# Performance work log

Hardware: AMD Instinct MI355X
Metric: run time of the kernel (lower is better)

## Reference

```python
import jax, jax.numpy as jnp
import numpy as np


def setup_inputs() -> dict:
    key = jax.random.key(0)
    ks = jax.random.split(key, 12)
    Tq, Tk, B, H = 1024, 1024, 8, 1024
    inp = {
        "inputs_q": jax.random.normal(ks[0], (Tq, B, H), jnp.float32),
        "inputs_kv": jax.random.normal(ks[1], (Tk, B, H), jnp.float32),
        "w_q": jax.random.normal(ks[2], (H, H), jnp.float32) * 0.02,
        "b_q": jnp.zeros((H,), jnp.float32),
        "w_kv": jax.random.normal(ks[3], (2 * H, H), jnp.float32) * 0.02,
        "b_kv": jnp.zeros((2 * H,), jnp.float32),
        "w_o": jax.random.normal(ks[4], (H, H), jnp.float32) * 0.02,
        "b_o": jnp.zeros((H,), jnp.float32),
        # BatchEnsemble rank-1 factors, initialized near 1
        "r_q": 1.0 + 0.05 * jax.random.normal(ks[5], (B, H), jnp.float32),
        "s_q": 1.0 + 0.05 * jax.random.normal(ks[6], (B, H), jnp.float32),
        "r_kv": 1.0 + 0.05 * jax.random.normal(ks[7], (B, H), jnp.float32),
        "s_kv": 1.0 + 0.05 * jax.random.normal(ks[8], (B, 2 * H), jnp.float32),
        "heads": 16,
    }
    return inp


def be_linear(x, w, b, r, s):
    # x: [T,B,Hin], w: [Hout,Hin], r: [B,Hin], s: [B,Hout]
    return jnp.einsum('tbh,oh->tbo', x * r, w) * s + b


def reference(inputs_q, inputs_kv, w_q, b_q, w_kv, b_kv, w_o, b_o,
              r_q, s_q, r_kv, s_kv, heads):
    Tq, B, H = inputs_q.shape
    Tk = inputs_kv.shape[0]
    hd = H // heads
    scale = hd ** -0.5

    q = be_linear(inputs_q, w_q, b_q, r_q, s_q)          # [Tq,B,H]
    kv = be_linear(inputs_kv, w_kv, b_kv, r_kv, s_kv)    # [Tk,B,2H]

    queries = q.reshape(Tq, B * heads, hd)
    kv = kv.reshape(Tk, B * heads, 2, hd)                # layout: head x {k,v} x hd
    keys = kv[:, :, 0, :]
    values = kv[:, :, 1, :]

    scores = jnp.einsum('qnd,knd->nqk', queries, keys) * scale  # [B*heads,Tq,Tk]
    probs = jax.nn.softmax(scores.astype(jnp.float32), axis=-1).astype(scores.dtype)
    # dropout_prob = 0 / eval: dropout is identity
    ctx = jnp.einsum('nqk,knd->qnd', probs, values).reshape(Tq, B, H)
    out = jnp.einsum('tbh,oh->tbo', ctx, w_o) + b_o      # [Tq,B,H]
    return out
```

## Files before the change

kernel.cpp:

```cpp
#include <hip/hip_runtime.h>
#include <stdint.h>

typedef unsigned short u16;
typedef __bf16 bf16x8 __attribute__((ext_vector_type(8)));
typedef float f32x4 __attribute__((ext_vector_type(4)));

typedef __attribute__((address_space(3))) void lds_void;
typedef const __attribute__((address_space(1))) void gbl_void;
#define GLD_LDS16(g, l) __builtin_amdgcn_global_load_lds((gbl_void*)(g), (lds_void*)(l), 16, 0, 0)

#define BAR_RELAX() asm volatile("s_waitcnt vmcnt(4)\n\ts_barrier" ::: "memory")
#define BAR_FULL()  asm volatile("s_waitcnt vmcnt(0)\n\ts_barrier" ::: "memory")

__device__ __forceinline__ u16 f2bf(float f) {
  unsigned u = __float_as_uint(f);
  u += 0x7fffu + ((u >> 16) & 1u);
  return (u16)(u >> 16);
}

__device__ __forceinline__ unsigned pk2bf(float a, float b) {
  unsigned au = __float_as_uint(a) + 0x8000u;
  unsigned bu = __float_as_uint(b) + 0x8000u;
  return __builtin_amdgcn_perm(bu, au, 0x07060302u);
}

__global__ void k_convert_all(const float* __restrict__ inq, const float* __restrict__ r_q,
                              const float* __restrict__ inkv, const float* __restrict__ r_kv,
                              const float* __restrict__ w_q, const float* __restrict__ w_kv,
                              const float* __restrict__ w_o,
                              u16* __restrict__ Xq, u16* __restrict__ Xkv,
                              u16* __restrict__ Wq, u16* __restrict__ Wkv,
                              u16* __restrict__ Wo) {
#pragma unroll 1
  for (int blk = blockIdx.x; blk < 20480; blk += 2560) {
    const float* src; const float* r = nullptr; u16* dst; int base;
    if (blk < 8192)       { src = inq;  r = r_q;  dst = Xq;  base = 0; }
    else if (blk < 16384) { src = inkv; r = r_kv; dst = Xkv; base = 8192; }
    else if (blk < 17408) { src = w_q;  dst = Wq;  base = 16384; }
    else if (blk < 19456) { src = w_kv; dst = Wkv; base = 17408; }
    else                  { src = w_o;  dst = Wo;  base = 19456; }
    int i4 = ((blk - base) * 256 + threadIdx.x) * 4;
    float4 xv = *(const float4*)(src + i4);
    if (r) {
      int rb = ((i4 >> 10) & 7) * 1024 + (i4 & 1023);
      float4 rv = *(const float4*)(r + rb);
      xv.x *= rv.x; xv.y *= rv.y; xv.z *= rv.z; xv.w *= rv.w;
    }
    unsigned long long pk = (unsigned long long)pk2bf(xv.x, xv.y)
        | ((unsigned long long)pk2bf(xv.z, xv.w) << 32);
    *(unsigned long long*)(dst + i4) = pk;
  }
}

template <int MODE>
__device__ __forceinline__ void gemm_tile(const u16* __restrict__ A, const u16* __restrict__ B,
                                          void* __restrict__ Cout, const float* __restrict__ s,
                                          const float* __restrict__ bias, int N, int K,
                                          float postscale, int bx, int by,
                                          u16* As, u16* Bs, int tid,
                                          u16* __restrict__ vt, int h) {
  const int w = tid >> 6, lane = tid & 63;
  const int quad = lane >> 4, l16 = lane & 15;
  const int n0 = bx * 128, m0 = by * 128;
  const int wm = (w & 1) * 64, wn = (w >> 1) * 64;

  f32x4 acc[4][4] = {};

  int srow[2], scol[2];
#pragma unroll
  for (int i = 0; i < 2; ++i) {
    int p = (w * 2 + i) * 64 + lane;
    int row = p >> 2;
    int cb = (p & 3) ^ ((row >> 1) & 3);
    srow[i] = row; scol[i] = cb * 8;
  }
  int offA[4], offB[4];
#pragma unroll
  for (int t = 0; t < 4; ++t) {
    int ra = wm + t * 16 + l16;
    offA[t] = ra * 32 + ((quad ^ ((ra >> 1) & 3)) * 8);
    int rb = wn + t * 16 + l16;
    offB[t] = rb * 32 + ((quad ^ ((rb >> 1) & 3)) * 8);
  }

#pragma unroll
  for (int st = 0; st < 2; ++st)
#pragma unroll
    for (int i = 0; i < 2; ++i) {
      GLD_LDS16(A + (size_t)(m0 + srow[i]) * K + st * 32 + scol[i],
                As + st * 4096 + (w * 2 + i) * 512);
      GLD_LDS16(B + (size_t)(n0 + srow[i]) * K + st * 32 + scol[i],
                Bs + st * 4096 + (w * 2 + i) * 512);
    }

  int cur = 0, nxt = 2;
#pragma unroll 1
  for (int k0 = 0; k0 < K; k0 += 32) {
    if (k0 + 32 >= K) BAR_FULL(); else BAR_RELAX();

    if (k0 + 64 < K) {
#pragma unroll
      for (int i = 0; i < 2; ++i) {
        GLD_LDS16(A + (size_t)(m0 + srow[i]) * K + (k0 + 64) + scol[i],
                  As + nxt * 4096 + (w * 2 + i) * 512);
        GLD_LDS16(B + (size_t)(n0 + srow[i]) * K + (k0 + 64) + scol[i],
                  Bs + nxt * 4096 + (w * 2 + i) * 512);
      }
    }
    const u16* Ac = As + cur * 4096;
    const u16* Bc = Bs + cur * 4096;
    bf16x8 af[4], bfr[4];
#pragma unroll
    for (int mt = 0; mt < 4; ++mt) af[mt] = *(const bf16x8*)(Ac + offA[mt]);
#pragma unroll
    for (int nt = 0; nt < 4; ++nt) bfr[nt] = *(const bf16x8*)(Bc + offB[nt]);
#pragma unroll
    for (int mt = 0; mt < 4; ++mt)
#pragma unroll
      for (int nt = 0; nt < 4; ++nt)
        acc[mt][nt] = __builtin_amdgcn_mfma_f32_16x16x32_bf16(bfr[nt], af[mt], acc[mt][nt], 0, 0, 0);
    cur = (cur == 2) ? 0 : cur + 1;
    nxt = (nxt == 2) ? 0 : nxt + 1;
  }

  if (MODE == 0) {
#pragma unroll
    for (int mt = 0; mt < 4; ++mt) {
      const int m = m0 + wm + mt * 16 + l16;
      const size_t rowb = (size_t)m * N;
      const float* srw = s + (m & 7) * N;
#pragma unroll
      for (int nt = 0; nt < 4; ++nt) {
        const int nb = n0 + wn + nt * 16 + quad * 4;
        float4 sv = *(const float4*)(srw + nb);
        float4 bv = *(const float4*)(bias + nb);
        f32x4 a = acc[mt][nt];
        unsigned long long pk =
            (unsigned long long)pk2bf((a[0] * sv.x + bv.x) * postscale,
                                      (a[1] * sv.y + bv.y) * postscale)
          | ((unsigned long long)pk2bf((a[2] * sv.z + bv.z) * postscale,
                                       (a[3] * sv.w + bv.w) * postscale) << 32);
        *(unsigned long long*)((u16*)Cout + rowb + nb) = pk;
      }
    }
  } else if (MODE == 1) {
#pragma unroll
    for (int mt = 0; mt < 4; ++mt) {
      const int m = m0 + wm + mt * 16 + l16;
      const size_t rowb = (size_t)m * N;
#pragma unroll
      for (int nt = 0; nt < 4; ++nt) {
        const int nb = n0 + wn + nt * 16 + quad * 4;
        float4 bv = *(const float4*)(bias + nb);
        f32x4 a = acc[mt][nt];
        float4 o = {a[0] + bv.x, a[1] + bv.y, a[2] + bv.z, a[3] + bv.w};
        *(float4*)((float*)Cout + rowb + nb) = o;
      }
    }
  } else {
    __syncthreads();
    if (wn == 0) {
#pragma unroll
      for (int mt = 0; mt < 4; ++mt) {
        const int m = m0 + wm + mt * 16 + l16;
        const int b = m & 7, tk = m >> 3;
        u16* krow = (u16*)Cout + ((size_t)(tk * 128 + b * 16 + h)) * 64;
        const float* srw = s + (m & 7) * N;
#pragma unroll
        for (int nt = 0; nt < 4; ++nt) {
          const int nb = n0 + nt * 16 + quad * 4;
          float4 sv = *(const float4*)(srw + nb);
          float4 bv = *(const float4*)(bias + nb);
          f32x4 a = acc[mt][nt];
          unsigned long long pk =
              (unsigned long long)pk2bf(a[0] * sv.x + bv.x, a[1] * sv.y + bv.y)
            | ((unsigned long long)pk2bf(a[2] * sv.z + bv.z, a[3] * sv.w + bv.w) << 32);
          *(unsigned long long*)(krow + nt * 16 + quad * 4) = pk;
        }
      }
    } else {
      u16* L = As + (w - 2) * 4608;
#pragma unroll
      for (int mt = 0; mt < 4; ++mt) {
        const int m = m0 + wm + mt * 16 + l16;
        const int b = m & 7;
        const int tkl = (mt * 16 + l16) >> 3;
        const float* srw = s + (m & 7) * N;
#pragma unroll
        for (int nt = 0; nt < 4; ++nt) {
          const int nb = n0 + 64 + nt * 16 + quad * 4;
          float4 sv = *(const float4*)(srw + nb);
          float4 bv = *(const float4*)(bias + nb);
          f32x4 a = acc[mt][nt];
          const int dl = nt * 16 + quad * 4;
          L[(dl + 0) * 72 + b * 8 + tkl] = f2bf(a[0] * sv.x + bv.x);
          L[(dl + 1) * 72 + b * 8 + tkl] = f2bf(a[1] * sv.y + bv.y);
          L[(dl + 2) * 72 + b * 8 + tkl] = f2bf(a[2] * sv.z + bv.z);
          L[(dl + 3) * 72 + b * 8 + tkl] = f2bf(a[3] * sv.w + bv.w);
        }
      }
      asm volatile("s_waitcnt lgkmcnt(0)" ::: "memory");
      const int tk0 = by * 16 + (wm >> 3);
#pragma unroll
      for (int it = 0; it < 8; ++it) {
        const int dloc = it * 8 + (lane >> 3);
        const int b = lane & 7;
        bf16x8 vchunk = *(const bf16x8*)(L + dloc * 72 + b * 8);
        *(bf16x8*)(vt + ((size_t)((b * 16 + h) * 64 + dloc)) * 1024 + tk0) = vchunk;
      }
    }
  }
}

__global__ void k_gemm_qkv(const u16* __restrict__ Xq, const u16* __restrict__ Wq,
                           u16* __restrict__ qout, const float* __restrict__ s_q,
                           const float* __restrict__ b_q, float qscale,
                           const u16* __restrict__ Xkv, const u16* __restrict__ Wkv,
                           u16* __restrict__ kbuf, const float* __restrict__ s_kv,
                           const float* __restrict__ b_kv, u16* __restrict__ vt) {
  __shared__ __align__(16) u16 As[3 * 4096];
  __shared__ __align__(16) u16 Bs[3 * 4096];
  const int blk = blockIdx.x;
  const int xcd = blk & 7;
  const int slot = blk >> 3;
  const int bx = slot % 24;
  const int by = xcd * 8 + slot / 24;
  if (bx < 8)
    gemm_tile<0>(Xq, Wq, qout, s_q, b_q, 1024, 1024, qscale, bx, by, As, Bs,
                 threadIdx.x, nullptr, 0);
  else
    gemm_tile<2>(Xkv, Wkv, kbuf, s_kv, b_kv, 2048, 1024, 1.0f, bx - 8, by, As, Bs,
                 threadIdx.x, vt, bx - 8);
}

__global__ void k_gemm_o(const u16* __restrict__ A, const u16* __restrict__ B,
                         float* __restrict__ Cout, const float* __restrict__ bias) {
  __shared__ __align__(16) u16 As[3 * 4096];
  __shared__ __align__(16) u16 Bs[3 * 4096];
  const int blk = blockIdx.x;
  const int xcd = blk & 7;
  const int slot = blk >> 3;
  const int bx = slot % 8;
  const int by = xcd * 8 + slot / 8;
  gemm_tile<1>(A, B, Cout, nullptr, bias, 1024, 1024, 1.0f, bx, by, As, Bs,
               threadIdx.x, nullptr, 0);
}

__global__ __launch_bounds__(256, 3) void k_attn(const u16* __restrict__ qb,
                                                 const u16* __restrict__ kb,
                                                 const u16* __restrict__ vtb,
                                                 u16* __restrict__ ctx) {
  __shared__ __align__(16) u16 Ks[2][4096];
  __shared__ __align__(16) u16 Vts[2][4096];
  __shared__ __align__(16) u16 Ps[4][32 * 72];

  const int tid = threadIdx.x;
  const int w = tid >> 6, lane = tid & 63;
  const int quad = lane >> 4, l16 = lane & 15;
  const int n = blockIdx.x & 127;
  const int q0 = (blockIdx.x >> 7) << 7;
  const int qw = q0 + w * 32;

  bf16x8 bq[2][2];
#pragma unroll
  for (int g = 0; g < 2; ++g)
#pragma unroll
    for (int ks = 0; ks < 2; ++ks)
      bq[g][ks] = *(const bf16x8*)(qb + ((size_t)(qw + g * 16 + l16) * 128 + n) * 64 + ks * 32 + quad * 8);

  const bool isK = (w < 2);
  const int wv = w & 1;
  const u16* gbase[4];
  u16* lbase[4];
#pragma unroll
  for (int i = 0; i < 4; ++i) {
    int p = (wv * 4 + i) * 64 + lane;
    int r = p >> 3;
    int scb = ((p & 7) ^ (r & 7)) * 8;
    if (isK) {
      gbase[i] = kb + ((size_t)r * 128 + n) * 64 + scb;
      lbase[i] = &Ks[0][(wv * 4 + i) * 512];
    } else {
      gbase[i] = vtb + ((size_t)n * 64 + r) * 1024 + scb;
      lbase[i] = &Vts[0][(wv * 4 + i) * 512];
    }
  }
  const size_t gstep = isK ? 8192 : 1;
  const int lstep = 4096;

  float l_i[2] = {0.f, 0.f};
  f32x4 accO[2][4] = {};
  u16* myP = Ps[w];

#pragma unroll
  for (int i = 0; i < 4; ++i) GLD_LDS16(gbase[i], lbase[i]);

#pragma unroll 1
  for (int tk0 = 0; tk0 < 1024; tk0 += 64) {
    const int cur = (tk0 >> 6) & 1;
    __syncthreads();
    if (tk0 < 960) {
      size_t goff = (size_t)(tk0 + 64) * gstep;
#pragma unroll
      for (int i = 0; i < 4; ++i)
        GLD_LDS16(gbase[i] + goff, lbase[i] + (cur ^ 1) * lstep);
    }
    const u16* Kc = Ks[cur];
    const u16* Vc = Vts[cur];

    f32x4 accS[2][4] = {};
#pragma unroll
    for (int mt = 0; mt < 4; ++mt) {
      int r = mt * 16 + l16;
#pragma unroll
      for (int ks = 0; ks < 2; ++ks) {
        bf16x8 ak = *(const bf16x8*)(Kc + r * 64 + (((ks * 4 + quad) ^ (r & 7)) << 3));
#pragma unroll
        for (int g = 0; g < 2; ++g)
          accS[g][mt] = __builtin_amdgcn_mfma_f32_16x16x32_bf16(ak, bq[g][ks], accS[g][mt], 0, 0, 0);
      }
    }

#pragma unroll
    for (int g = 0; g < 2; ++g) {
      float pv[16];
      float ss = 0.f;
#pragma unroll
      for (int mt = 0; mt < 4; ++mt)
#pragma unroll
        for (int rg = 0; rg < 4; ++rg) {
          float p = __builtin_amdgcn_exp2f(accS[g][mt][rg]);
          pv[mt * 4 + rg] = p;
          ss += p;
        }
      ss += __shfl_xor(ss, 16);
      ss += __shfl_xor(ss, 32);
      l_i[g] += ss;
      const int prow = (g * 16 + l16) * 72;
#pragma unroll
      for (int mt = 0; mt < 4; ++mt) {
        unsigned long long pk = (unsigned long long)pk2bf(pv[mt * 4 + 0], pv[mt * 4 + 1])
            | ((unsigned long long)pk2bf(pv[mt * 4 + 2], pv[mt * 4 + 3]) << 32);
        *(unsigned long long*)(myP + prow + mt * 16 + quad * 4) = pk;
      }
    }

    bf16x8 bp[2][2];
#pragma unroll
    for (int g = 0; g < 2; ++g)
#pragma unroll
      for (int ks = 0; ks < 2; ++ks)
        bp[g][ks] = *(const bf16x8*)(myP + (g * 16 + l16) * 72 + ks * 32 + quad * 8);
#pragma unroll
    for (int dt = 0; dt < 4; ++dt) {
      int r = dt * 16 + l16;
#pragma unroll
      for (int ks = 0; ks < 2; ++ks) {
        bf16x8 av = *(const bf16x8*)(Vc + r * 64 + (((ks * 4 + quad) ^ (r & 7)) << 3));
#pragma unroll
        for (int g = 0; g < 2; ++g)
          accO[g][dt] = __builtin_amdgcn_mfma_f32_16x16x32_bf16(av, bp[g][ks], accO[g][dt], 0, 0, 0);
      }
    }
  }

#pragma unroll
  for (int g = 0; g < 2; ++g) {
    float inv = 1.f / l_i[g];
    const size_t obase = ((size_t)(qw + g * 16 + l16) * 128 + n) * 64;
#pragma unroll
    for (int dt = 0; dt < 4; ++dt) {
      unsigned long long pk = (unsigned long long)pk2bf(accO[g][dt][0] * inv, accO[g][dt][1] * inv)
          | ((unsigned long long)pk2bf(accO[g][dt][2] * inv, accO[g][dt][3] * inv) << 32);
      *(unsigned long long*)(ctx + obase + dt * 16 + quad * 4) = pk;
    }
  }
}

extern "C" void kernel_launch(void* const* d_in, const int* in_sizes, int n_in,
                              void* d_out, int out_size, void* d_ws, size_t ws_size,
                              hipStream_t stream) {
  const float* inq  = (const float*)d_in[0];
  const float* inkv = (const float*)d_in[1];
  const float* w_q  = (const float*)d_in[2];
  const float* b_q  = (const float*)d_in[3];
  const float* w_kv = (const float*)d_in[4];
  const float* b_kv = (const float*)d_in[5];
  const float* w_o  = (const float*)d_in[6];
  const float* b_o  = (const float*)d_in[7];
  const float* r_q  = (const float*)d_in[8];
  const float* s_q  = (const float*)d_in[9];
  const float* r_kv = (const float*)d_in[10];
  const float* s_kv = (const float*)d_in[11];

  const size_t MEG = 1024 * 1024;
  u16* ws    = (u16*)d_ws;
  u16* Xq    = ws;
  u16* Xkv   = ws + 8 * MEG;
  u16* Wq    = ws + 16 * MEG;
  u16* Wkv   = ws + 17 * MEG;
  u16* Wo    = ws + 19 * MEG;
  u16* qbuf  = ws + 20 * MEG;
  u16* kbuf  = ws + 28 * MEG;
  u16* vt    = ws + 36 * MEG;
  u16* ctx   = Xq;

  k_convert_all<<<2560, 256, 0, stream>>>(inq, r_q, inkv, r_kv, w_q, w_kv, w_o,
                                          Xq, Xkv, Wq, Wkv, Wo);

  const float QSCALE = 0.125f * 1.44269504088896340736f;
  k_gemm_qkv<<<1536, 256, 0, stream>>>(Xq, Wq, qbuf, s_q, b_q, QSCALE,
                                       Xkv, Wkv, kbuf, s_kv, b_kv, vt);
  k_attn<<<1024, 256, 0, stream>>>(qbuf, kbuf, vt, ctx);
  k_gemm_o<<<512, 256, 0, stream>>>(ctx, Wo, (float*)d_out, b_o);
}
```

Measured before the change: 290.0 us.

## Use 256x128 tiles in the fused QKV projection GEMM

The QKV projection GEMM now uses 256-row by 128-column output tiles, with 8x4 MFMA accumulators per wave, instead of 128x128, which halves the grid to 768 blocks. The A-tile loads, the barrier wait count and the V-transpose epilogue (LDS staging stride and store pattern) are adjusted to match. The aim is to reuse the B tile across more rows and cut global and LDS traffic per flop. In exchange it uses more registers and LDS, which may lower occupancy, and fewer blocks may leave the wave tail less balanced.

```diff
diff --git a/kernel.cpp b/kernel.cpp
--- a/kernel.cpp
+++ b/kernel.cpp
@@ -9,8 +9,9 @@
 typedef const __attribute__((address_space(1))) void gbl_void;
 #define GLD_LDS16(g, l) __builtin_amdgcn_global_load_lds((gbl_void*)(g), (lds_void*)(l), 16, 0, 0)
 
-#define BAR_RELAX() asm volatile("s_waitcnt vmcnt(4)\n\ts_barrier" ::: "memory")
-#define BAR_FULL()  asm volatile("s_waitcnt vmcnt(0)\n\ts_barrier" ::: "memory")
+#define BAR_RELAX()  asm volatile("s_waitcnt vmcnt(4)\n\ts_barrier" ::: "memory")
+#define BAR_RELAX6() asm volatile("s_waitcnt vmcnt(6)\n\ts_barrier" ::: "memory")
+#define BAR_FULL()   asm volatile("s_waitcnt vmcnt(0)\n\ts_barrier" ::: "memory")
 
 __device__ __forceinline__ u16 f2bf(float f) {
   unsigned u = __float_as_uint(f);
@@ -53,69 +54,81 @@
 }
 
 template <int MODE>
-__device__ __forceinline__ void gemm_tile(const u16* __restrict__ A, const u16* __restrict__ B,
-                                          void* __restrict__ Cout, const float* __restrict__ s,
-                                          const float* __restrict__ bias, int N, int K,
-                                          float postscale, int bx, int by,
-                                          u16* As, u16* Bs, int tid,
-                                          u16* __restrict__ vt, int h) {
+__device__ __forceinline__ void gemm_tile_w128(const u16* __restrict__ A, const u16* __restrict__ B,
+                                               void* __restrict__ Cout, const float* __restrict__ s,
+                                               const float* __restrict__ bias, int N, int K,
+                                               float postscale, int bx, int by,
+                                               u16* As, u16* Bs, int tid,
+                                               u16* __restrict__ vt, int h) {
   const int w = tid >> 6, lane = tid & 63;
   const int quad = lane >> 4, l16 = lane & 15;
-  const int n0 = bx * 128, m0 = by * 128;
-  const int wm = (w & 1) * 64, wn = (w >> 1) * 64;
-
-  f32x4 acc[4][4] = {};
-
-  int srow[2], scol[2];
+  const int n0 = bx * 128, m0 = by * 256;
+  const int wm = (w & 1) * 128, wn = (w >> 1) * 64;
+
+  f32x4 acc[8][4] = {};
+
+  int arow[4], acol[4];
+#pragma unroll
+  for (int i = 0; i < 4; ++i) {
+    int p = (w * 4 + i) * 64 + lane;
+    arow[i] = p >> 2;
+    acol[i] = ((p & 3) ^ ((arow[i] >> 1) & 3)) * 8;
+  }
+  int brow[2], bcol[2];
 #pragma unroll
   for (int i = 0; i < 2; ++i) {
     int p = (w * 2 + i) * 64 + lane;
-    int row = p >> 2;
-    int cb = (p & 3) ^ ((row >> 1) & 3);
-    srow[i] = row; scol[i] = cb * 8;
-  }
-  int offA[4], offB[4];
-#pragma unroll
-  for (int t = 0; t < 4; ++t) {
+    brow[i] = p >> 2;
+    bcol[i] = ((p & 3) ^ ((brow[i] >> 1) & 3)) * 8;
+  }
+  int offA[8], offB[4];
+#pragma unroll
+  for (int t = 0; t < 8; ++t) {
     int ra = wm + t * 16 + l16;
     offA[t] = ra * 32 + ((quad ^ ((ra >> 1) & 3)) * 8);
+  }
+#pragma unroll
+  for (int t = 0; t < 4; ++t) {
     int rb = wn + t * 16 + l16;
     offB[t] = rb * 32 + ((quad ^ ((rb >> 1) & 3)) * 8);
   }
 
 #pragma unroll
-  for (int st = 0; st < 2; ++st)
-#pragma unroll
-    for (int i = 0; i < 2; ++i) {
-      GLD_LDS16(A + (size_t)(m0 + srow[i]) * K + st * 32 + scol[i],
-                As + st * 4096 + (w * 2 + i) * 512);
-      GLD_LDS16(B + (size_t)(n0 + srow[i]) * K + st * 32 + scol[i],
+  for (int st = 0; st < 2; ++st) {
+#pragma unroll
+    for (int i = 0; i < 4; ++i)
+      GLD_LDS16(A + (size_t)(m0 + arow[i]) * K + st * 32 + acol[i],
+                As + st * 8192 + (w * 4 + i) * 512);
+#pragma unroll
+    for (int i = 0; i < 2; ++i)
+      GLD_LDS16(B + (size_t)(n0 + brow[i]) * K + st * 32 + bcol[i],
                 Bs + st * 4096 + (w * 2 + i) * 512);
-    }
+  }
 
   int cur = 0, nxt = 2;
 #pragma unroll 1
   for (int k0 = 0; k0 < K; k0 += 32) {
-    if (k0 + 32 >= K) BAR_FULL(); else BAR_RELAX();
+    if (k0 + 32 >= K) BAR_FULL(); else BAR_RELAX6();
 
     if (k0 + 64 < K) {
 #pragma unroll
-      for (int i = 0; i < 2; ++i) {
-        GLD_LDS16(A + (size_t)(m0 + srow[i]) * K + (k0 + 64) + scol[i],
-                  As + nxt * 4096 + (w * 2 + i) * 512);
-        GLD_LDS16(B + (size_t)(n0 + srow[i]) * K + (k0 + 64) + scol[i],
+      for (int i = 0; i < 4; ++i)
+        GLD_LDS16(A + (size_t)(m0 + arow[i]) * K + (k0 + 64) + acol[i],
+                  As + nxt * 8192 + (w * 4 + i) * 512);
+#pragma unroll
+      for (int i = 0; i < 2; ++i)
+        GLD_LDS16(B + (size_t)(n0 + brow[i]) * K + (k0 + 64) + bcol[i],
                   Bs + nxt * 4096 + (w * 2 + i) * 512);
-      }
-    }
-    const u16* Ac = As + cur * 4096;
+    }
+    const u16* Ac = As + cur * 8192;
     const u16* Bc = Bs + cur * 4096;
-    bf16x8 af[4], bfr[4];
-#pragma unroll
-    for (int mt = 0; mt < 4; ++mt) af[mt] = *(const bf16x8*)(Ac + offA[mt]);
+    bf16x8 af[8], bfr[4];
+#pragma unroll
+    for (int mt = 0; mt < 8; ++mt) af[mt] = *(const bf16x8*)(Ac + offA[mt]);
 #pragma unroll
     for (int nt = 0; nt < 4; ++nt) bfr[nt] = *(const bf16x8*)(Bc + offB[nt]);
 #pragma unroll
-    for (int mt = 0; mt < 4; ++mt)
+    for (int mt = 0; mt < 8; ++mt)
 #pragma unroll
       for (int nt = 0; nt < 4; ++nt)
         acc[mt][nt] = __builtin_amdgcn_mfma_f32_16x16x32_bf16(bfr[nt], af[mt], acc[mt][nt], 0, 0, 0);
@@ -125,7 +138,7 @@
 
   if (MODE == 0) {
 #pragma unroll
-    for (int mt = 0; mt < 4; ++mt) {
+    for (int mt = 0; mt < 8; ++mt) {
       const int m = m0 + wm + mt * 16 + l16;
       const size_t rowb = (size_t)m * N;
       const float* srw = s + (m & 7) * N;
@@ -143,25 +156,11 @@
         *(unsigned long long*)((u16*)Cout + rowb + nb) = pk;
       }
     }
-  } else if (MODE == 1) {
-#pragma unroll
-    for (int mt = 0; mt < 4; ++mt) {
-      const int m = m0 + wm + mt * 16 + l16;
-      const size_t rowb = (size_t)m * N;
-#pragma unroll
-      for (int nt = 0; nt < 4; ++nt) {
-        const int nb = n0 + wn + nt * 16 + quad * 4;
-        float4 bv = *(const float4*)(bias + nb);
-        f32x4 a = acc[mt][nt];
-        float4 o = {a[0] + bv.x, a[1] + bv.y, a[2] + bv.z, a[3] + bv.w};
-        *(float4*)((float*)Cout + rowb + nb) = o;
-      }
-    }
   } else {
     __syncthreads();
     if (wn == 0) {
 #pragma unroll
-      for (int mt = 0; mt < 4; ++mt) {
+      for (int mt = 0; mt < 8; ++mt) {
         const int m = m0 + wm + mt * 16 + l16;
         const int b = m & 7, tk = m >> 3;
         u16* krow = (u16*)Cout + ((size_t)(tk * 128 + b * 16 + h)) * 64;
@@ -179,9 +178,9 @@
         }
       }
     } else {
-      u16* L = As + (w - 2) * 4608;
-#pragma unroll
-      for (int mt = 0; mt < 4; ++mt) {
+      u16* L = As + (w - 2) * 8704;
+#pragma unroll
+      for (int mt = 0; mt < 8; ++mt) {
         const int m = m0 + wm + mt * 16 + l16;
         const int b = m & 7;
         const int tkl = (mt * 16 + l16) >> 3;
@@ -193,44 +192,132 @@
           float4 bv = *(const float4*)(bias + nb);
           f32x4 a = acc[mt][nt];
           const int dl = nt * 16 + quad * 4;
-          L[(dl + 0) * 72 + b * 8 + tkl] = f2bf(a[0] * sv.x + bv.x);
-          L[(dl + 1) * 72 + b * 8 + tkl] = f2bf(a[1] * sv.y + bv.y);
-          L[(dl + 2) * 72 + b * 8 + tkl] = f2bf(a[2] * sv.z + bv.z);
-          L[(dl + 3) * 72 + b * 8 + tkl] = f2bf(a[3] * sv.w + bv.w);
+          L[(dl + 0) * 136 + b * 16 + tkl] = f2bf(a[0] * sv.x + bv.x);
+          L[(dl + 1) * 136 + b * 16 + tkl] = f2bf(a[1] * sv.y + bv.y);
+          L[(dl + 2) * 136 + b * 16 + tkl] = f2bf(a[2] * sv.z + bv.z);
+          L[(dl + 3) * 136 + b * 16 + tkl] = f2bf(a[3] * sv.w + bv.w);
         }
       }
       asm volatile("s_waitcnt lgkmcnt(0)" ::: "memory");
-      const int tk0 = by * 16 + (wm >> 3);
-#pragma unroll
-      for (int it = 0; it < 8; ++it) {
-        const int dloc = it * 8 + (lane >> 3);
-        const int b = lane & 7;
-        bf16x8 vchunk = *(const bf16x8*)(L + dloc * 72 + b * 8);
-        *(bf16x8*)(vt + ((size_t)((b * 16 + h) * 64 + dloc)) * 1024 + tk0) = vchunk;
-      }
-    }
-  }
-}
-
-__global__ void k_gemm_qkv(const u16* __restrict__ Xq, const u16* __restrict__ Wq,
-                           u16* __restrict__ qout, const float* __restrict__ s_q,
-                           const float* __restrict__ b_q, float qscale,
-                           const u16* __restrict__ Xkv, const u16* __restrict__ Wkv,
-                           u16* __restrict__ kbuf, const float* __restrict__ s_kv,
-                           const float* __restrict__ b_kv, u16* __restrict__ vt) {
-  __shared__ __align__(16) u16 As[3 * 4096];
+      const int tk0w = by * 32 + (wm >> 3);
+#pragma unroll
+      for (int it = 0; it < 16; ++it) {
+        const int dloc = it * 4 + (lane >> 4);
+        const int b = (lane >> 1) & 7;
+        const int th = lane & 1;
+        bf16x8 vchunk = *(const bf16x8*)(L + dloc * 136 + b * 16 + th * 8);
+        *(bf16x8*)(vt + ((size_t)((b * 16 + h) * 64 + dloc)) * 1024 + tk0w + th * 8) = vchunk;
+      }
+    }
+  }
+}
+
+__global__ void k_gemm_qkv(
+    const u16* __restrict__ Xq, const u16* __restrict__ Wq,
+    u16* __restrict__ qout, const float* __restrict__ s_q,
+    const float* __restrict__ b_q, float qscale,
+    const u16* __restrict__ Xkv, const u16* __restrict__ Wkv,
+    u16* __restrict__ kbuf, const float* __restrict__ s_kv,
+    const float* __restrict__ b_kv, u16* __restrict__ vt) {
+  __shared__ __align__(16) u16 As[3 * 8192];
   __shared__ __align__(16) u16 Bs[3 * 4096];
   const int blk = blockIdx.x;
   const int xcd = blk & 7;
   const int slot = blk >> 3;
-  const int bx = slot % 24;
-  const int by = xcd * 8 + slot / 24;
-  if (bx < 8)
-    gemm_tile<0>(Xq, Wq, qout, s_q, b_q, 1024, 1024, qscale, bx, by, As, Bs,
-                 threadIdx.x, nullptr, 0);
+  const int by = xcd * 4 + slot / 24;
+  const int cx = slot % 24;
+  if (cx < 8)
+    gemm_tile_w128<0>(Xq, Wq, qout, s_q, b_q, 1024, 1024, qscale, cx, by, As, Bs,
+                      threadIdx.x, nullptr, 0);
   else
-    gemm_tile<2>(Xkv, Wkv, kbuf, s_kv, b_kv, 2048, 1024, 1.0f, bx - 8, by, As, Bs,
-                 threadIdx.x, vt, bx - 8);
+    gemm_tile_w128<2>(Xkv, Wkv, kbuf, s_kv, b_kv, 2048, 1024, 1.0f, cx - 8, by, As, Bs,
+                      threadIdx.x, vt, cx - 8);
+}
+
+template <int MODE>
+__device__ __forceinline__ void gemm_tile(const u16* __restrict__ A, const u16* __restrict__ B,
+                                          void* __restrict__ Cout, const float* __restrict__ s,
+                                          const float* __restrict__ bias, int N, int K,
+                                          float postscale, int bx, int by,
+                                          u16* As, u16* Bs, int tid,
+                                          u16* __restrict__ vt, int h) {
+  const int w = tid >> 6, lane = tid & 63;
+  const int quad = lane >> 4, l16 = lane & 15;
+  const int n0 = bx * 128, m0 = by * 128;
+  const int wm = (w & 1) * 64, wn = (w >> 1) * 64;
+
+  f32x4 acc[4][4] = {};
+
+  int srow[2], scol[2];
+#pragma unroll
+  for (int i = 0; i < 2; ++i) {
+    int p = (w * 2 + i) * 64 + lane;
+    int row = p >> 2;
+    int cb = (p & 3) ^ ((row >> 1) & 3);
+    srow[i] = row; scol[i] = cb * 8;
+  }
+  int offA[4], offB[4];
+#pragma unroll
+  for (int t = 0; t < 4; ++t) {
+    int ra = wm + t * 16 + l16;
+    offA[t] = ra * 32 + ((quad ^ ((ra >> 1) & 3)) * 8);
+    int rb = wn + t * 16 + l16;
+    offB[t] = rb * 32 + ((quad ^ ((rb >> 1) & 3)) * 8);
+  }
+
+#pragma unroll
+  for (int st = 0; st < 2; ++st)
+#pragma unroll
+    for (int i = 0; i < 2; ++i) {
+      GLD_LDS16(A + (size_t)(m0 + srow[i]) * K + st * 32 + scol[i],
+                As + st * 4096 + (w * 2 + i) * 512);
+      GLD_LDS16(B + (size_t)(n0 + srow[i]) * K + st * 32 + scol[i],
+                Bs + st * 4096 + (w * 2 + i) * 512);
+    }
+
+  int cur = 0, nxt = 2;
+#pragma unroll 1
+  for (int k0 = 0; k0 < K; k0 += 32) {
+    if (k0 + 32 >= K) BAR_FULL(); else BAR_RELAX();
+
+    if (k0 + 64 < K) {
+#pragma unroll
+      for (int i = 0; i < 2; ++i) {
+        GLD_LDS16(A + (size_t)(m0 + srow[i]) * K + (k0 + 64) + scol[i],
+                  As + nxt * 4096 + (w * 2 + i) * 512);
+        GLD_LDS16(B + (size_t)(n0 + srow[i]) * K + (k0 + 64) + scol[i],
+                  Bs + nxt * 4096 + (w * 2 + i) * 512);
+      }
+    }
+    const u16* Ac = As + cur * 4096;
+    const u16* Bc = Bs + cur * 4096;
+    bf16x8 af[4], bfr[4];
+#pragma unroll
+    for (int mt = 0; mt < 4; ++mt) af[mt] = *(const bf16x8*)(Ac + offA[mt]);
+#pragma unroll
+    for (int nt = 0; nt < 4; ++nt) bfr[nt] = *(const bf16x8*)(Bc + offB[nt]);
+#pragma unroll
+    for (int mt = 0; mt < 4; ++mt)
+#pragma unroll
+      for (int nt = 0; nt < 4; ++nt)
+        acc[mt][nt] = __builtin_amdgcn_mfma_f32_16x16x32_bf16(bfr[nt], af[mt], acc[mt][nt], 0, 0, 0);
+    cur = (cur == 2) ? 0 : cur + 1;
+    nxt = (nxt == 2) ? 0 : nxt + 1;
+  }
+
+#pragma unroll
+  for (int mt = 0; mt < 4; ++mt) {
+    const int m = m0 + wm + mt * 16 + l16;
+    const size_t rowb = (size_t)m * N;
+#pragma unroll
+    for (int nt = 0; nt < 4; ++nt) {
+      const int nb = n0 + wn + nt * 16 + quad * 4;
+      float4 bv = *(const float4*)(bias + nb);
+      f32x4 a = acc[mt][nt];
+      float4 o = {a[0] + bv.x, a[1] + bv.y, a[2] + bv.z, a[3] + bv.w};
+      *(float4*)((float*)Cout + rowb + nb) = o;
+    }
+  }
 }
 
 __global__ void k_gemm_o(const u16* __restrict__ A, const u16* __restrict__ B,
@@ -409,8 +496,8 @@
                                           Xq, Xkv, Wq, Wkv, Wo);
 
   const float QSCALE = 0.125f * 1.44269504088896340736f;
-  k_gemm_qkv<<<1536, 256, 0, stream>>>(Xq, Wq, qbuf, s_q, b_q, QSCALE,
-                                       Xkv, Wkv, kbuf, s_kv, b_kv, vt);
+  k_gemm_qkv<<<768, 256, 0, stream>>>(Xq, Wq, qbuf, s_q, b_q, QSCALE,
+                                      Xkv, Wkv, kbuf, s_kv, b_kv, vt);
   k_attn<<<1024, 256, 0, stream>>>(qbuf, kbuf, vt, ctx);
   k_gemm_o<<<512, 256, 0, stream>>>(ctx, Wo, (float*)d_out, b_o);
 }
```

New measurement: 679.2 us. +134.2%, slower.

## Use single-buffered BK=64 tiles with 3-block occupancy in QKV GEMM

Applied to the files above, without the earlier changes.

The QKV projection GEMM now uses a single-stage 64-wide K tile with a new XOR swizzle and two MFMA sub-steps per barrier, in place of the triple-buffered 32-wide pipeline. LDS per block shrinks to 32KB and launch bounds request three blocks per CU, so latency is hidden by occupancy rather than in-block prefetch. It also halves the number of loop iterations and barriers. The risk is exposed load latency, since each tile waits on a full vmcnt(0) before compute. The output GEMM keeps the old pipelined path.

```diff
diff --git a/kernel.cpp b/kernel.cpp
--- a/kernel.cpp
+++ b/kernel.cpp
@@ -11,6 +11,7 @@
 
 #define BAR_RELAX() asm volatile("s_waitcnt vmcnt(4)\n\ts_barrier" ::: "memory")
 #define BAR_FULL()  asm volatile("s_waitcnt vmcnt(0)\n\ts_barrier" ::: "memory")
+#define BAR()       asm volatile("s_barrier" ::: "memory")
 
 __device__ __forceinline__ u16 f2bf(float f) {
   unsigned u = __float_as_uint(f);
@@ -53,12 +54,12 @@
 }
 
 template <int MODE>
-__device__ __forceinline__ void gemm_tile(const u16* __restrict__ A, const u16* __restrict__ B,
-                                          void* __restrict__ Cout, const float* __restrict__ s,
-                                          const float* __restrict__ bias, int N, int K,
-                                          float postscale, int bx, int by,
-                                          u16* As, u16* Bs, int tid,
-                                          u16* __restrict__ vt, int h) {
+__device__ __forceinline__ void gemm_tile64(const u16* __restrict__ A, const u16* __restrict__ B,
+                                            void* __restrict__ Cout, const float* __restrict__ s,
+                                            const float* __restrict__ bias, int N, int K,
+                                            float postscale, int bx, int by,
+                                            u16* As, u16* Bs, int tid,
+                                            u16* __restrict__ vt, int h) {
   const int w = tid >> 6, lane = tid & 63;
   const int quad = lane >> 4, l16 = lane & 15;
   const int n0 = bx * 128, m0 = by * 128;
@@ -66,61 +67,53 @@
 
   f32x4 acc[4][4] = {};
 
-  int srow[2], scol[2];
-#pragma unroll
-  for (int i = 0; i < 2; ++i) {
-    int p = (w * 2 + i) * 64 + lane;
-    int row = p >> 2;
-    int cb = (p & 3) ^ ((row >> 1) & 3);
-    srow[i] = row; scol[i] = cb * 8;
-  }
+  const int srow_in = lane >> 3;
+  const int scb = ((lane & 7) ^ srow_in) * 8;
   int offA[4], offB[4];
 #pragma unroll
   for (int t = 0; t < 4; ++t) {
     int ra = wm + t * 16 + l16;
-    offA[t] = ra * 32 + ((quad ^ ((ra >> 1) & 3)) * 8);
+    offA[t] = ra * 64 + ((quad ^ (ra & 7)) << 3);
     int rb = wn + t * 16 + l16;
-    offB[t] = rb * 32 + ((quad ^ ((rb >> 1) & 3)) * 8);
-  }
-
-#pragma unroll
-  for (int st = 0; st < 2; ++st)
-#pragma unroll
-    for (int i = 0; i < 2; ++i) {
-      GLD_LDS16(A + (size_t)(m0 + srow[i]) * K + st * 32 + scol[i],
-                As + st * 4096 + (w * 2 + i) * 512);
-      GLD_LDS16(B + (size_t)(n0 + srow[i]) * K + st * 32 + scol[i],
-                Bs + st * 4096 + (w * 2 + i) * 512);
-    }
-
-  int cur = 0, nxt = 2;
+    offB[t] = rb * 64 + ((quad ^ (rb & 7)) << 3);
+  }
+
+#pragma unroll
+  for (int i = 0; i < 4; ++i) {
+    const int ai = w * 4 + i;
+    GLD_LDS16(A + (size_t)(m0 + ai * 8 + srow_in) * K + scb, As + ai * 512);
+    GLD_LDS16(B + (size_t)(n0 + ai * 8 + srow_in) * K + scb, Bs + ai * 512);
+  }
+
 #pragma unroll 1
-  for (int k0 = 0; k0 < K; k0 += 32) {
-    if (k0 + 32 >= K) BAR_FULL(); else BAR_RELAX();
-
+  for (int k0 = 0; k0 < K; k0 += 64) {
+    BAR_FULL();
+
+#pragma unroll
+    for (int ks = 0; ks < 2; ++ks) {
+      const int kx = ks << 5;
+      bf16x8 af[4], bfr[4];
+#pragma unroll
+      for (int t = 0; t < 4; ++t) {
+        af[t]  = *(const bf16x8*)(As + (offA[t] ^ kx));
+        bfr[t] = *(const bf16x8*)(Bs + (offB[t] ^ kx));
+      }
+#pragma unroll
+      for (int mt = 0; mt < 4; ++mt)
+#pragma unroll
+        for (int nt = 0; nt < 4; ++nt)
+          acc[mt][nt] = __builtin_amdgcn_mfma_f32_16x16x32_bf16(bfr[nt], af[mt], acc[mt][nt], 0, 0, 0);
+    }
+
+    BAR();
     if (k0 + 64 < K) {
 #pragma unroll
-      for (int i = 0; i < 2; ++i) {
-        GLD_LDS16(A + (size_t)(m0 + srow[i]) * K + (k0 + 64) + scol[i],
-                  As + nxt * 4096 + (w * 2 + i) * 512);
-        GLD_LDS16(B + (size_t)(n0 + srow[i]) * K + (k0 + 64) + scol[i],
-                  Bs + nxt * 4096 + (w * 2 + i) * 512);
-      }
-    }
-    const u16* Ac = As + cur * 4096;
-    const u16* Bc = Bs + cur * 4096;
-    bf16x8 af[4], bfr[4];
-#pragma unroll
-    for (int mt = 0; mt < 4; ++mt) af[mt] = *(const bf16x8*)(Ac + offA[mt]);
-#pragma unroll
-    for (int nt = 0; nt < 4; ++nt) bfr[nt] = *(const bf16x8*)(Bc + offB[nt]);
-#pragma unroll
-    for (int mt = 0; mt < 4; ++mt)
-#pragma unroll
-      for (int nt = 0; nt < 4; ++nt)
-        acc[mt][nt] = __builtin_amdgcn_mfma_f32_16x16x32_bf16(bfr[nt], af[mt], acc[mt][nt], 0, 0, 0);
-    cur = (cur == 2) ? 0 : cur + 1;
-    nxt = (nxt == 2) ? 0 : nxt + 1;
+      for (int i = 0; i < 4; ++i) {
+        const int ai = w * 4 + i;
+        GLD_LDS16(A + (size_t)(m0 + ai * 8 + srow_in) * K + (k0 + 64) + scb, As + ai * 512);
+        GLD_LDS16(B + (size_t)(n0 + ai * 8 + srow_in) * K + (k0 + 64) + scb, Bs + ai * 512);
+      }
+    }
   }
 
   if (MODE == 0) {
@@ -143,20 +136,6 @@
         *(unsigned long long*)((u16*)Cout + rowb + nb) = pk;
       }
     }
-  } else if (MODE == 1) {
-#pragma unroll
-    for (int mt = 0; mt < 4; ++mt) {
-      const int m = m0 + wm + mt * 16 + l16;
-      const size_t rowb = (size_t)m * N;
-#pragma unroll
-      for (int nt = 0; nt < 4; ++nt) {
-        const int nb = n0 + wn + nt * 16 + quad * 4;
-        float4 bv = *(const float4*)(bias + nb);
-        f32x4 a = acc[mt][nt];
-        float4 o = {a[0] + bv.x, a[1] + bv.y, a[2] + bv.z, a[3] + bv.w};
-        *(float4*)((float*)Cout + rowb + nb) = o;
-      }
-    }
   } else {
     __syncthreads();
     if (wn == 0) {
@@ -179,7 +158,7 @@
         }
       }
     } else {
-      u16* L = As + (w - 2) * 4608;
+      u16* L = (w == 2) ? As : Bs;
 #pragma unroll
       for (int mt = 0; mt < 4; ++mt) {
         const int m = m0 + wm + mt * 16 + l16;
@@ -212,25 +191,112 @@
   }
 }
 
-__global__ void k_gemm_qkv(const u16* __restrict__ Xq, const u16* __restrict__ Wq,
-                           u16* __restrict__ qout, const float* __restrict__ s_q,
-                           const float* __restrict__ b_q, float qscale,
-                           const u16* __restrict__ Xkv, const u16* __restrict__ Wkv,
-                           u16* __restrict__ kbuf, const float* __restrict__ s_kv,
-                           const float* __restrict__ b_kv, u16* __restrict__ vt) {
-  __shared__ __align__(16) u16 As[3 * 4096];
-  __shared__ __align__(16) u16 Bs[3 * 4096];
+__global__ __launch_bounds__(256, 3) void k_gemm_qkv(
+    const u16* __restrict__ Xq, const u16* __restrict__ Wq,
+    u16* __restrict__ qout, const float* __restrict__ s_q,
+    const float* __restrict__ b_q, float qscale,
+    const u16* __restrict__ Xkv, const u16* __restrict__ Wkv,
+    u16* __restrict__ kbuf, const float* __restrict__ s_kv,
+    const float* __restrict__ b_kv, u16* __restrict__ vt) {
+  __shared__ __align__(16) u16 As[8192];
+  __shared__ __align__(16) u16 Bs[8192];
   const int blk = blockIdx.x;
   const int xcd = blk & 7;
   const int slot = blk >> 3;
   const int bx = slot % 24;
   const int by = xcd * 8 + slot / 24;
   if (bx < 8)
-    gemm_tile<0>(Xq, Wq, qout, s_q, b_q, 1024, 1024, qscale, bx, by, As, Bs,
-                 threadIdx.x, nullptr, 0);
+    gemm_tile64<0>(Xq, Wq, qout, s_q, b_q, 1024, 1024, qscale, bx, by, As, Bs,
+                   threadIdx.x, nullptr, 0);
   else
-    gemm_tile<2>(Xkv, Wkv, kbuf, s_kv, b_kv, 2048, 1024, 1.0f, bx - 8, by, As, Bs,
-                 threadIdx.x, vt, bx - 8);
+    gemm_tile64<2>(Xkv, Wkv, kbuf, s_kv, b_kv, 2048, 1024, 1.0f, bx - 8, by, As, Bs,
+                   threadIdx.x, vt, bx - 8);
+}
+
+template <int MODE>
+__device__ __forceinline__ void gemm_tile(const u16* __restrict__ A, const u16* __restrict__ B,
+                                          void* __restrict__ Cout, const float* __restrict__ s,
+                                          const float* __restrict__ bias, int N, int K,
+                                          float postscale, int bx, int by,
+                                          u16* As, u16* Bs, int tid,
+                                          u16* __restrict__ vt, int h) {
+  const int w = tid >> 6, lane = tid & 63;
+  const int quad = lane >> 4, l16 = lane & 15;
+  const int n0 = bx * 128, m0 = by * 128;
+  const int wm = (w & 1) * 64, wn = (w >> 1) * 64;
+
+  f32x4 acc[4][4] = {};
+
+  int srow[2], scol[2];
+#pragma unroll
+  for (int i = 0; i < 2; ++i) {
+    int p = (w * 2 + i) * 64 + lane;
+    int row = p >> 2;
+    int cb = (p & 3) ^ ((row >> 1) & 3);
+    srow[i] = row; scol[i] = cb * 8;
+  }
+  int offA[4], offB[4];
+#pragma unroll
+  for (int t = 0; t < 4; ++t) {
+    int ra = wm + t * 16 + l16;
+    offA[t] = ra * 32 + ((quad ^ ((ra >> 1) & 3)) * 8);
+    int rb = wn + t * 16 + l16;
+    offB[t] = rb * 32 + ((quad ^ ((rb >> 1) & 3)) * 8);
+  }
+
+#pragma unroll
+  for (int st = 0; st < 2; ++st)
+#pragma unroll
+    for (int i = 0; i < 2; ++i) {
+      GLD_LDS16(A + (size_t)(m0 + srow[i]) * K + st * 32 + scol[i],
+                As + st * 4096 + (w * 2 + i) * 512);
+      GLD_LDS16(B + (size_t)(n0 + srow[i]) * K + st * 32 + scol[i],
+                Bs + st * 4096 + (w * 2 + i) * 512);
+    }
+
+  int cur = 0, nxt = 2;
+#pragma unroll 1
+  for (int k0 = 0; k0 < K; k0 += 32) {
+    if (k0 + 32 >= K) BAR_FULL(); else BAR_RELAX();
+
+    if (k0 + 64 < K) {
+#pragma unroll
+      for (int i = 0; i < 2; ++i) {
+        GLD_LDS16(A + (size_t)(m0 + srow[i]) * K + (k0 + 64) + scol[i],
+                  As + nxt * 4096 + (w * 2 + i) * 512);
+        GLD_LDS16(B + (size_t)(n0 + srow[i]) * K + (k0 + 64) + scol[i],
+                  Bs + nxt * 4096 + (w * 2 + i) * 512);
+      }
+    }
+    const u16* Ac = As + cur * 4096;
+    const u16* Bc = Bs + cur * 4096;
+    bf16x8 af[4], bfr[4];
+#pragma unroll
+    for (int mt = 0; mt < 4; ++mt) af[mt] = *(const bf16x8*)(Ac + offA[mt]);
+#pragma unroll
+    for (int nt = 0; nt < 4; ++nt) bfr[nt] = *(const bf16x8*)(Bc + offB[nt]);
+#pragma unroll
+    for (int mt = 0; mt < 4; ++mt)
+#pragma unroll
+      for (int nt = 0; nt < 4; ++nt)
+        acc[mt][nt] = __builtin_amdgcn_mfma_f32_16x16x32_bf16(bfr[nt], af[mt], acc[mt][nt], 0, 0, 0);
+    cur = (cur == 2) ? 0 : cur + 1;
+    nxt = (nxt == 2) ? 0 : nxt + 1;
+  }
+
+#pragma unroll
+  for (int mt = 0; mt < 4; ++mt) {
+    const int m = m0 + wm + mt * 16 + l16;
+    const size_t rowb = (size_t)m * N;
+#pragma unroll
+    for (int nt = 0; nt < 4; ++nt) {
+      const int nb = n0 + wn + nt * 16 + quad * 4;
+      float4 bv = *(const float4*)(bias + nb);
+      f32x4 a = acc[mt][nt];
+      float4 o = {a[0] + bv.x, a[1] + bv.y, a[2] + bv.z, a[3] + bv.w};
+      *(float4*)((float*)Cout + rowb + nb) = o;
+    }
+  }
 }
 
 __global__ void k_gemm_o(const u16* __restrict__ A, const u16* __restrict__ B,
```

Result: no change. 291.0 us (+0.3%).

## Single-buffer LDS in GEMM and attention to raise occupancy, swizzle P tile

Applied to the files above, without the earlier changes.

The GEMM tile drops its 3-stage BK=32 LDS ring for a single BK=64 buffer with an XOR swizzle, and gets launch bounds of 3 blocks per CU. The attention kernel drops double-buffered K/V tiles for single buffers and swizzles the P scratch tile with a 64-wide stride instead of a padded 72 stride, letting it target 4 blocks per CU. The aim is to cut LDS use so more blocks fit per CU and hide latency that way. The cost is that each global load now waits on a full barrier and no longer overlaps with compute inside a block.

```diff
diff --git a/kernel.cpp b/kernel.cpp
--- a/kernel.cpp
+++ b/kernel.cpp
@@ -9,8 +9,8 @@
 typedef const __attribute__((address_space(1))) void gbl_void;
 #define GLD_LDS16(g, l) __builtin_amdgcn_global_load_lds((gbl_void*)(g), (lds_void*)(l), 16, 0, 0)
 
-#define BAR_RELAX() asm volatile("s_waitcnt vmcnt(4)\n\ts_barrier" ::: "memory")
 #define BAR_FULL()  asm volatile("s_waitcnt vmcnt(0)\n\ts_barrier" ::: "memory")
+#define BAR()       asm volatile("s_barrier" ::: "memory")
 
 __device__ __forceinline__ u16 f2bf(float f) {
   unsigned u = __float_as_uint(f);
@@ -53,12 +53,12 @@
 }
 
 template <int MODE>
-__device__ __forceinline__ void gemm_tile(const u16* __restrict__ A, const u16* __restrict__ B,
-                                          void* __restrict__ Cout, const float* __restrict__ s,
-                                          const float* __restrict__ bias, int N, int K,
-                                          float postscale, int bx, int by,
-                                          u16* As, u16* Bs, int tid,
-                                          u16* __restrict__ vt, int h) {
+__device__ __forceinline__ void gemm_tile64(const u16* __restrict__ A, const u16* __restrict__ B,
+                                            void* __restrict__ Cout, const float* __restrict__ s,
+                                            const float* __restrict__ bias, int N, int K,
+                                            float postscale, int bx, int by,
+                                            u16* As, u16* Bs, int tid,
+                                            u16* __restrict__ vt, int h) {
   const int w = tid >> 6, lane = tid & 63;
   const int quad = lane >> 4, l16 = lane & 15;
   const int n0 = bx * 128, m0 = by * 128;
@@ -66,61 +66,53 @@
 
   f32x4 acc[4][4] = {};
 
-  int srow[2], scol[2];
-#pragma unroll
-  for (int i = 0; i < 2; ++i) {
-    int p = (w * 2 + i) * 64 + lane;
-    int row = p >> 2;
-    int cb = (p & 3) ^ ((row >> 1) & 3);
-    srow[i] = row; scol[i] = cb * 8;
-  }
+  const int srow_in = lane >> 3;
+  const int scb = ((lane & 7) ^ srow_in) * 8;
   int offA[4], offB[4];
 #pragma unroll
   for (int t = 0; t < 4; ++t) {
     int ra = wm + t * 16 + l16;
-    offA[t] = ra * 32 + ((quad ^ ((ra >> 1) & 3)) * 8);
+    offA[t] = ra * 64 + ((quad ^ (ra & 7)) << 3);
     int rb = wn + t * 16 + l16;
-    offB[t] = rb * 32 + ((quad ^ ((rb >> 1) & 3)) * 8);
-  }
-
-#pragma unroll
-  for (int st = 0; st < 2; ++st)
-#pragma unroll
-    for (int i = 0; i < 2; ++i) {
-      GLD_LDS16(A + (size_t)(m0 + srow[i]) * K + st * 32 + scol[i],
-                As + st * 4096 + (w * 2 + i) * 512);
-      GLD_LDS16(B + (size_t)(n0 + srow[i]) * K + st * 32 + scol[i],
-                Bs + st * 4096 + (w * 2 + i) * 512);
-    }
-
-  int cur = 0, nxt = 2;
+    offB[t] = rb * 64 + ((quad ^ (rb & 7)) << 3);
+  }
+
+#pragma unroll
+  for (int i = 0; i < 4; ++i) {
+    const int ai = w * 4 + i;
+    GLD_LDS16(A + (size_t)(m0 + ai * 8 + srow_in) * K + scb, As + ai * 512);
+    GLD_LDS16(B + (size_t)(n0 + ai * 8 + srow_in) * K + scb, Bs + ai * 512);
+  }
+
 #pragma unroll 1
-  for (int k0 = 0; k0 < K; k0 += 32) {
-    if (k0 + 32 >= K) BAR_FULL(); else BAR_RELAX();
-
+  for (int k0 = 0; k0 < K; k0 += 64) {
+    BAR_FULL();
+
+#pragma unroll
+    for (int ks = 0; ks < 2; ++ks) {
+      const int kx = ks << 5;
+      bf16x8 af[4], bfr[4];
+#pragma unroll
+      for (int t = 0; t < 4; ++t) {
+        af[t]  = *(const bf16x8*)(As + (offA[t] ^ kx));
+        bfr[t] = *(const bf16x8*)(Bs + (offB[t] ^ kx));
+      }
+#pragma unroll
+      for (int mt = 0; mt < 4; ++mt)
+#pragma unroll
+        for (int nt = 0; nt < 4; ++nt)
+          acc[mt][nt] = __builtin_amdgcn_mfma_f32_16x16x32_bf16(bfr[nt], af[mt], acc[mt][nt], 0, 0, 0);
+    }
+
+    BAR();
     if (k0 + 64 < K) {
 #pragma unroll
-      for (int i = 0; i < 2; ++i) {
-        GLD_LDS16(A + (size_t)(m0 + srow[i]) * K + (k0 + 64) + scol[i],
-                  As + nxt * 4096 + (w * 2 + i) * 512);
-        GLD_LDS16(B + (size_t)(n0 + srow[i]) * K + (k0 + 64) + scol[i],
-                  Bs + nxt * 4096 + (w * 2 + i) * 512);
-      }
-    }
-    const u16* Ac = As + cur * 4096;
-    const u16* Bc = Bs + cur * 4096;
-    bf16x8 af[4], bfr[4];
-#pragma unroll
-    for (int mt = 0; mt < 4; ++mt) af[mt] = *(const bf16x8*)(Ac + offA[mt]);
-#pragma unroll
-    for (int nt = 0; nt < 4; ++nt) bfr[nt] = *(const bf16x8*)(Bc + offB[nt]);
-#pragma unroll
-    for (int mt = 0; mt < 4; ++mt)
-#pragma unroll
-      for (int nt = 0; nt < 4; ++nt)
-        acc[mt][nt] = __builtin_amdgcn_mfma_f32_16x16x32_bf16(bfr[nt], af[mt], acc[mt][nt], 0, 0, 0);
-    cur = (cur == 2) ? 0 : cur + 1;
-    nxt = (nxt == 2) ? 0 : nxt + 1;
+      for (int i = 0; i < 4; ++i) {
+        const int ai = w * 4 + i;
+        GLD_LDS16(A + (size_t)(m0 + ai * 8 + srow_in) * K + (k0 + 64) + scb, As + ai * 512);
+        GLD_LDS16(B + (size_t)(n0 + ai * 8 + srow_in) * K + (k0 + 64) + scb, Bs + ai * 512);
+      }
+    }
   }
 
   if (MODE == 0) {
@@ -179,7 +171,7 @@
         }
       }
     } else {
-      u16* L = As + (w - 2) * 4608;
+      u16* L = (w == 2) ? As : Bs;
 #pragma unroll
       for (int mt = 0; mt < 4; ++mt) {
         const int m = m0 + wm + mt * 16 + l16;
@@ -212,47 +204,49 @@
   }
 }
 
-__global__ void k_gemm_qkv(const u16* __restrict__ Xq, const u16* __restrict__ Wq,
-                           u16* __restrict__ qout, const float* __restrict__ s_q,
-                           const float* __restrict__ b_q, float qscale,
-                           const u16* __restrict__ Xkv, const u16* __restrict__ Wkv,
-                           u16* __restrict__ kbuf, const float* __restrict__ s_kv,
-                           const float* __restrict__ b_kv, u16* __restrict__ vt) {
-  __shared__ __align__(16) u16 As[3 * 4096];
-  __shared__ __align__(16) u16 Bs[3 * 4096];
+__global__ __launch_bounds__(256, 3) void k_gemm_qkv(
+    const u16* __restrict__ Xq, const u16* __restrict__ Wq,
+    u16* __restrict__ qout, const float* __restrict__ s_q,
+    const float* __restrict__ b_q, float qscale,
+    const u16* __restrict__ Xkv, const u16* __restrict__ Wkv,
+    u16* __restrict__ kbuf, const float* __restrict__ s_kv,
+    const float* __restrict__ b_kv, u16* __restrict__ vt) {
+  __shared__ __align__(16) u16 As[8192];
+  __shared__ __align__(16) u16 Bs[8192];
   const int blk = blockIdx.x;
   const int xcd = blk & 7;
   const int slot = blk >> 3;
   const int bx = slot % 24;
   const int by = xcd * 8 + slot / 24;
   if (bx < 8)
-    gemm_tile<0>(Xq, Wq, qout, s_q, b_q, 1024, 1024, qscale, bx, by, As, Bs,
-                 threadIdx.x, nullptr, 0);
+    gemm_tile64<0>(Xq, Wq, qout, s_q, b_q, 1024, 1024, qscale, bx, by, As, Bs,
+                   threadIdx.x, nullptr, 0);
   else
-    gemm_tile<2>(Xkv, Wkv, kbuf, s_kv, b_kv, 2048, 1024, 1.0f, bx - 8, by, As, Bs,
-                 threadIdx.x, vt, bx - 8);
-}
-
-__global__ void k_gemm_o(const u16* __restrict__ A, const u16* __restrict__ B,
-                         float* __restrict__ Cout, const float* __restrict__ bias) {
-  __shared__ __align__(16) u16 As[3 * 4096];
-  __shared__ __align__(16) u16 Bs[3 * 4096];
+    gemm_tile64<2>(Xkv, Wkv, kbuf, s_kv, b_kv, 2048, 1024, 1.0f, bx - 8, by, As, Bs,
+                   threadIdx.x, vt, bx - 8);
+}
+
+__global__ __launch_bounds__(256, 3) void k_gemm_o(
+    const u16* __restrict__ A, const u16* __restrict__ B,
+    float* __restrict__ Cout, const float* __restrict__ bias) {
+  __shared__ __align__(16) u16 As[8192];
+  __shared__ __align__(16) u16 Bs[8192];
   const int blk = blockIdx.x;
   const int xcd = blk & 7;
   const int slot = blk >> 3;
   const int bx = slot % 8;
   const int by = xcd * 8 + slot / 8;
-  gemm_tile<1>(A, B, Cout, nullptr, bias, 1024, 1024, 1.0f, bx, by, As, Bs,
-               threadIdx.x, nullptr, 0);
-}
-
-__global__ __launch_bounds__(256, 3) void k_attn(const u16* __restrict__ qb,
+  gemm_tile64<1>(A, B, Cout, nullptr, bias, 1024, 1024, 1.0f, bx, by, As, Bs,
+                 threadIdx.x, nullptr, 0);
+}
+
+__global__ __launch_bounds__(256, 4) void k_attn(const u16* __restrict__ qb,
                                                  const u16* __restrict__ kb,
                                                  const u16* __restrict__ vtb,
                                                  u16* __restrict__ ctx) {
-  __shared__ __align__(16) u16 Ks[2][4096];
-  __shared__ __align__(16) u16 Vts[2][4096];
-  __shared__ __align__(16) u16 Ps[4][32 * 72];
+  __shared__ __align__(16) u16 Ks[4096];
+  __shared__ __align__(16) u16 Vts[4096];
+  __shared__ __align__(16) u16 Ps[4][32 * 64];
 
   const int tid = threadIdx.x;
   const int w = tid >> 6, lane = tid & 63;
@@ -279,34 +273,25 @@
     int scb = ((p & 7) ^ (r & 7)) * 8;
     if (isK) {
       gbase[i] = kb + ((size_t)r * 128 + n) * 64 + scb;
-      lbase[i] = &Ks[0][(wv * 4 + i) * 512];
+      lbase[i] = &Ks[(wv * 4 + i) * 512];
     } else {
       gbase[i] = vtb + ((size_t)n * 64 + r) * 1024 + scb;
-      lbase[i] = &Vts[0][(wv * 4 + i) * 512];
+      lbase[i] = &Vts[(wv * 4 + i) * 512];
     }
   }
   const size_t gstep = isK ? 8192 : 1;
-  const int lstep = 4096;
 
   float l_i[2] = {0.f, 0.f};
   f32x4 accO[2][4] = {};
   u16* myP = Ps[w];
+  const int pswz = l16 & 7;
 
 #pragma unroll
   for (int i = 0; i < 4; ++i) GLD_LDS16(gbase[i], lbase[i]);
 
 #pragma unroll 1
   for (int tk0 = 0; tk0 < 1024; tk0 += 64) {
-    const int cur = (tk0 >> 6) & 1;
-    __syncthreads();
-    if (tk0 < 960) {
-      size_t goff = (size_t)(tk0 + 64) * gstep;
-#pragma unroll
-      for (int i = 0; i < 4; ++i)
-        GLD_LDS16(gbase[i] + goff, lbase[i] + (cur ^ 1) * lstep);
-    }
-    const u16* Kc = Ks[cur];
-    const u16* Vc = Vts[cur];
+    BAR_FULL();
 
     f32x4 accS[2][4] = {};
 #pragma unroll
@@ -314,7 +299,7 @@
       int r = mt * 16 + l16;
 #pragma unroll
       for (int ks = 0; ks < 2; ++ks) {
-        bf16x8 ak = *(const bf16x8*)(Kc + r * 64 + (((ks * 4 + quad) ^ (r & 7)) << 3));
+        bf16x8 ak = *(const bf16x8*)(Ks + r * 64 + (((ks * 4 + quad) ^ (r & 7)) << 3));
 #pragma unroll
         for (int g = 0; g < 2; ++g)
           accS[g][mt] = __builtin_amdgcn_mfma_f32_16x16x32_bf16(ak, bq[g][ks], accS[g][mt], 0, 0, 0);
@@ -323,26 +308,23 @@
 
 #pragma unroll
     for (int g = 0; g < 2; ++g) {
-      float pv[16];
       float ss = 0.f;
-#pragma unroll
-      for (int mt = 0; mt < 4; ++mt)
-#pragma unroll
-        for (int rg = 0; rg < 4; ++rg) {
-          float p = __builtin_amdgcn_exp2f(accS[g][mt][rg]);
-          pv[mt * 4 + rg] = p;
-          ss += p;
-        }
+      const int prow = (g * 16 + l16) << 6;
+#pragma unroll
+      for (int mt = 0; mt < 4; ++mt) {
+        float p0 = __builtin_amdgcn_exp2f(accS[g][mt][0]);
+        float p1 = __builtin_amdgcn_exp2f(accS[g][mt][1]);
+        float p2 = __builtin_amdgcn_exp2f(accS[g][mt][2]);
+        float p3 = __builtin_amdgcn_exp2f(accS[g][mt][3]);
+        ss += (p0 + p1) + (p2 + p3);
+        unsigned long long pk = (unsigned long long)pk2bf(p0, p1)
+            | ((unsigned long long)pk2bf(p2, p3) << 32);
+        *(unsigned long long*)(myP + prow + ((((mt << 1) + (quad >> 1)) ^ pswz) << 3)
+                               + ((quad & 1) << 2)) = pk;
+      }
       ss += __shfl_xor(ss, 16);
       ss += __shfl_xor(ss, 32);
       l_i[g] += ss;
-      const int prow = (g * 16 + l16) * 72;
-#pragma unroll
-      for (int mt = 0; mt < 4; ++mt) {
-        unsigned long long pk = (unsigned long long)pk2bf(pv[mt * 4 + 0], pv[mt * 4 + 1])
-            | ((unsigned long long)pk2bf(pv[mt * 4 + 2], pv[mt * 4 + 3]) << 32);
-        *(unsigned long long*)(myP + prow + mt * 16 + quad * 4) = pk;
-      }
     }
 
     bf16x8 bp[2][2];
@@ -350,17 +332,27 @@
     for (int g = 0; g < 2; ++g)
 #pragma unroll
       for (int ks = 0; ks < 2; ++ks)
-        bp[g][ks] = *(const bf16x8*)(myP + (g * 16 + l16) * 72 + ks * 32 + quad * 8);
+        bp[g][ks] = *(const bf16x8*)(myP + ((g * 16 + l16) << 6)
+                                     + ((((ks << 2) + quad) ^ pswz) << 3));
+
 #pragma unroll
     for (int dt = 0; dt < 4; ++dt) {
       int r = dt * 16 + l16;
 #pragma unroll
       for (int ks = 0; ks < 2; ++ks) {
-        bf16x8 av = *(const bf16x8*)(Vc + r * 64 + (((ks * 4 + quad) ^ (r & 7)) << 3));
+        bf16x8 av = *(const bf16x8*)(Vts + r * 64 + (((ks * 4 + quad) ^ (r & 7)) << 3));
 #pragma unroll
         for (int g = 0; g < 2; ++g)
           accO[g][dt] = __builtin_amdgcn_mfma_f32_16x16x32_bf16(av, bp[g][ks], accO[g][dt], 0, 0, 0);
       }
+    }
+
+    BAR();
+    if (tk0 < 960) {
+      size_t goff = (size_t)(tk0 + 64) * gstep;
+#pragma unroll
+      for (int i = 0; i < 4; ++i)
+        GLD_LDS16(gbase[i] + goff, lbase[i]);
     }
   }
 
```

After: 288.0 us. About the same (-0.7%).
